# Kernel optimization log

Measured on AMD Instinct MI355X. Metric: run time of the kernel, lower is better.

The kernel has to match this reference:

```python
import jax, jax.numpy as jnp
import numpy as np
from jax import lax

R = 0.7          # ball-query radius
K = 32           # max neighbors per ball
STRIDE = 32      # spatial stride -> M = N // STRIDE anchors
COUT = 1024      # mlp_planes[0]


def fps(pts, M):
    """Furthest point sampling. pts: [N,3] -> int32 [M] indices (starts at 0, like CUDA FPS)."""
    N = pts.shape[0]

    def step(carry, _):
        d2, last = carry
        dist = jnp.sum((pts - pts[last]) ** 2, axis=-1)
        d2 = jnp.minimum(d2, dist)
        return (d2, jnp.argmax(d2).astype(jnp.int32)), last

    init = (jnp.full((N,), 1e10, dtype=pts.dtype), jnp.int32(0))
    _, idxs = lax.scan(step, init, None, length=M)
    return idxs


def ball_query(neigh, anchor):
    """neigh: [N,3], anchor: [M,3] -> int32 [M,K]: first K in-radius neighbor indices,
    padded with the first valid index (matching pointnet2 ball_query semantics)."""
    N = neigh.shape[0]
    d2 = jnp.sum((anchor[:, None, :] - neigh[None, :, :]) ** 2, axis=-1)  # [M,N]
    key = jnp.where(d2 < R * R, jnp.arange(N), N)  # valid points keep their position
    order = jnp.argsort(key, axis=-1)[:, :K]       # stable: first-in-order valid indices
    valid = jnp.take_along_axis(key, order, axis=-1) < N
    return jnp.where(valid, order, order[:, :1])


def setup_inputs() -> dict:
    key = jax.random.key(0)
    k1, k2 = jax.random.split(key)
    xyzs = jax.random.uniform(k1, (4, 16, 2048, 3), dtype=jnp.float32)  # points in unit cube
    w_d = jax.random.normal(k2, (COUT, 4), dtype=jnp.float32) * 0.1     # conv_d 1x1 weight
    return {"xyzs": xyzs, "w_d": w_d}


def reference(xyzs, w_d):
    B, T, N, _ = xyzs.shape
    M = N // STRIDE
    # replicate temporal padding [1,1]
    pad = jnp.concatenate([xyzs[:, :1], xyzs, xyzs[:, -1:]], axis=1)  # [B,T+2,N,3]

    anchors_src = pad[:, 1:-1].reshape(B * T, N, 3)
    aidx = jax.vmap(lambda p: fps(p, M))(anchors_src)                         # [BT,M]
    anchor = jnp.take_along_axis(anchors_src, aidx[..., None], axis=1)        # [BT,M,3]

    feat = None
    for dt in (-1, 0, 1):  # temporal kernel taps
        neigh = pad[:, 1 + dt: 1 + dt + T].reshape(B * T, N, 3)
        idx = jax.vmap(ball_query)(neigh, anchor)                             # [BT,M,K]
        grouped = jnp.take_along_axis(
            neigh, idx.reshape(B * T, M * K)[..., None], axis=1
        ).reshape(B * T, M, K, 3)
        disp = grouped - anchor[:, :, None, :]                                # xyz displacement
        d4 = jnp.concatenate(
            [disp, jnp.full((B * T, M, K, 1), float(dt), disp.dtype)], axis=-1
        )                                                                     # [BT,M,K,4]
        f = jax.nn.relu(jnp.einsum('nmkc,oc->nmko', d4, w_d))                 # 1x1 conv + ReLU
        f = jnp.max(f, axis=2)                                                # spatial max pool -> [BT,M,C]
        feat = f if feat is None else feat + f                                # temporal sum pool

    new_xyzs = anchor.reshape(B, T, M, 3)
    new_features = feat.reshape(B, T, M, COUT).transpose(0, 1, 3, 2)          # [B,T,C,M]
    return new_xyzs, new_features
```

## Files before the change

kernel.cpp:

```cpp
#include <hip/hip_runtime.h>
#include <hip/hip_fp16.h>

#define NB 4
#define NT 16
#define NN 2048
#define NM 64
#define NK 32
#define NC 1024

static __device__ inline __half2 h2max(__half2 a, __half2 b) {
    unsigned int ai = *(unsigned int*)&a, bi = *(unsigned int*)&b, di;
    asm("v_pk_max_f16 %0, %1, %2" : "=v"(di) : "v"(ai), "v"(bi));
    return *(__half2*)&di;
}

#define DPP_MAX_STEP(v, ctrl)                                                   \
    do {                                                                        \
        const int _mv = __builtin_amdgcn_update_dpp(                            \
            __float_as_int(v), __float_as_int(v), (ctrl), 0xf, 0xf, false);     \
        (v) = fmaxf((v), __int_as_float(_mv));                                  \
    } while (0)

static __device__ inline float readlane_f(float x, int l) {
    return __int_as_float(__builtin_amdgcn_readlane(__float_as_int(x), l));
}

__global__ __launch_bounds__(256) void fps_kernel(const float* __restrict__ xyzs,
                                                  float* __restrict__ out_xyz) {
    const int bt = blockIdx.x;
    const float* pts = xyzs + (size_t)bt * NN * 3;
    __shared__ unsigned long long sKey[2][4];
    __shared__ __align__(16) float sCand[2][4][4];
    __shared__ float sAnchor[NM * 3];
    __shared__ float sInit[3];
    const int tid = threadIdx.x;
    const int lane = tid & 63, wave = tid >> 6;
    float wpt[24];
    {
        const float4* pv = (const float4*)pts + (size_t)tid * 6;
        #pragma unroll
        for (int i = 0; i < 6; ++i) {
            const float4 f = pv[i];
            wpt[4 * i + 0] = f.x; wpt[4 * i + 1] = f.y; wpt[4 * i + 2] = f.z; wpt[4 * i + 3] = f.w;
        }
    }
    float px[8], py[8], pz[8], d2v[8];
    #pragma unroll
    for (int j = 0; j < 8; ++j) {
        px[j] = wpt[3 * j + 0]; py[j] = wpt[3 * j + 1]; pz[j] = wpt[3 * j + 2];
        d2v[j] = 1e10f;
    }
    if (tid == 0) { sInit[0] = px[0]; sInit[1] = py[0]; sInit[2] = pz[0]; }
    __syncthreads();
    float ax = sInit[0], ay = sInit[1], az = sInit[2];
    for (int it = 0; it < NM; ++it) {
        if (tid == 0) {
            sAnchor[it * 3 + 0] = ax; sAnchor[it * 3 + 1] = ay; sAnchor[it * 3 + 2] = az;
        }
        float bv = -1.0f; int bj = 0;
        #pragma unroll
        for (int j = 0; j < 8; ++j) {
            const float dx = __fsub_rn(px[j], ax), dy = __fsub_rn(py[j], ay), dz = __fsub_rn(pz[j], az);
            const float d = __fadd_rn(__fadd_rn(__fmul_rn(dx, dx), __fmul_rn(dy, dy)), __fmul_rn(dz, dz));
            d2v[j] = fminf(d2v[j], d);
            if (d2v[j] > bv) { bv = d2v[j]; bj = j; }
        }
        float v = bv;
        DPP_MAX_STEP(v, 0x111);
        DPP_MAX_STEP(v, 0x112);
        DPP_MAX_STEP(v, 0x114);
        DPP_MAX_STEP(v, 0x118);
        DPP_MAX_STEP(v, 0x142);
        DPP_MAX_STEP(v, 0x143);
        const float vmax = readlane_f(v, 63);
        const unsigned long long tied = __ballot(bv == vmax);
        const int src = (int)(__ffsll((long long)tied) - 1);
        const float cx0 = (bj & 1) ? px[1] : px[0], cx1 = (bj & 1) ? px[3] : px[2];
        const float cx2 = (bj & 1) ? px[5] : px[4], cx3 = (bj & 1) ? px[7] : px[6];
        const float cy0 = (bj & 1) ? py[1] : py[0], cy1 = (bj & 1) ? py[3] : py[2];
        const float cy2 = (bj & 1) ? py[5] : py[4], cy3 = (bj & 1) ? py[7] : py[6];
        const float cz0 = (bj & 1) ? pz[1] : pz[0], cz1 = (bj & 1) ? pz[3] : pz[2];
        const float cz2 = (bj & 1) ? pz[5] : pz[4], cz3 = (bj & 1) ? pz[7] : pz[6];
        const float cxa = (bj & 2) ? cx1 : cx0, cxb = (bj & 2) ? cx3 : cx2;
        const float cya = (bj & 2) ? cy1 : cy0, cyb = (bj & 2) ? cy3 : cy2;
        const float cza = (bj & 2) ? cz1 : cz0, czb = (bj & 2) ? cz3 : cz2;
        const float cx = (bj & 4) ? cxb : cxa;
        const float cy = (bj & 4) ? cyb : cya;
        const float cz = (bj & 4) ? czb : cza;
        const int idx = tid * 8 + bj;
        const int widx = __builtin_amdgcn_readlane(idx, src);
        const float wx = readlane_f(cx, src);
        const float wy = readlane_f(cy, src);
        const float wz = readlane_f(cz, src);
        const int par = it & 1;
        if (lane == 0) {
            sKey[par][wave] = ((unsigned long long)__float_as_uint(vmax) << 32)
                            | (unsigned)(NN - 1 - widx);
            *(float4*)&sCand[par][wave][0] = make_float4(wx, wy, wz, 0.0f);
        }
        __syncthreads();
        unsigned long long bk = sKey[par][0];
        float4 bc = *(const float4*)&sCand[par][0][0];
        #pragma unroll
        for (int i = 1; i < 4; ++i) {
            const unsigned long long ki = sKey[par][i];
            const float4 ci = *(const float4*)&sCand[par][i][0];
            if (ki > bk) { bk = ki; bc = ci; }
        }
        ax = bc.x; ay = bc.y; az = bc.z;
    }
    __syncthreads();
    for (int i = tid; i < NM * 3; i += 256)
        out_xyz[bt * NM * 3 + i] = sAnchor[i];
}

__global__ __launch_bounds__(256) void bq_kernel(const float* __restrict__ xyzs,
                                                 const float* __restrict__ anchors,
                                                 unsigned int* __restrict__ disp) {
    const int tid = threadIdx.x;
    const int lane = tid & 63, w = tid >> 6;
    const int q = blockIdx.x * 4 + w;
    const int bt = q / (NM * 3);
    const int r = q - bt * (NM * 3);
    const int m = r / 3, tap = r - m * 3;
    const int b = bt >> 4, t = bt & 15;
    __shared__ float sD[4][3][NK];
    const float ax = anchors[(bt * NM + m) * 3 + 0];
    const float ay = anchors[(bt * NM + m) * 3 + 1];
    const float az = anchors[(bt * NM + m) * 3 + 2];
    int tsrc = t + tap - 1;
    tsrc = tsrc < 0 ? 0 : (tsrc > NT - 1 ? NT - 1 : tsrc);
    const float* npts = xyzs + ((size_t)(b * NT + tsrc)) * NN * 3;
    int cnt = 0;
    for (int rr = 0; rr < NN / 64 && cnt < NK; ++rr) {
        const int n = rr * 64 + lane;
        const float dx = __fsub_rn(npts[n * 3 + 0], ax);
        const float dy = __fsub_rn(npts[n * 3 + 1], ay);
        const float dz = __fsub_rn(npts[n * 3 + 2], az);
        const float d2v = __fadd_rn(__fadd_rn(__fmul_rn(dx, dx), __fmul_rn(dy, dy)), __fmul_rn(dz, dz));
        const bool valid = d2v < 0.49f;
        const unsigned long long mask = __ballot(valid);
        const int pos = cnt + (int)__popcll(mask & ((1ull << lane) - 1ull));
        if (valid && pos < NK) {
            sD[w][0][pos] = dx; sD[w][1][pos] = dy; sD[w][2][pos] = dz;
        }
        cnt += (int)__popcll(mask);
    }
    if (cnt < NK) {
        float fx, fy, fz;
        if (cnt > 0) {
            fx = sD[w][0][0]; fy = sD[w][1][0]; fz = sD[w][2][0];
        } else {
            fx = __fsub_rn(npts[0], ax); fy = __fsub_rn(npts[1], ay); fz = __fsub_rn(npts[2], az);
        }
        if (lane >= cnt && lane < NK) {
            sD[w][0][lane] = fx; sD[w][1][lane] = fy; sD[w][2][lane] = fz;
        }
    }
    if (lane < 48) {
        const int c = lane >> 4, j = lane & 15;
        const __half2 hv = __float22half2_rn(make_float2(sD[w][c][2 * j], sD[w][c][2 * j + 1]));
        disp[(size_t)q * 48 + lane] = *(const unsigned int*)&hv;
    }
}

__global__ __launch_bounds__(256, 8) void conv_kernel(const unsigned int* __restrict__ disp,
                                                      const float* __restrict__ wd,
                                                      float* __restrict__ feat) {
    const int blk = blockIdx.x;
    const int bt = blk >> 5;
    const int inner = blk & 31;
    const int mh = inner >> 2, cq = inner & 3;
    const int tid = threadIdx.x;
    const int lane = tid & 63, w = tid >> 6;
    const int m0 = mh * 8 + w * 2;
    const int c0 = cq * 256 + lane;
    __half2 wx[4], wy[4], wz[4]; float ww[4];
    #pragma unroll
    for (int r = 0; r < 4; ++r) {
        const float4 wv = ((const float4*)wd)[c0 + 64 * r];
        wx[r] = __float2half2_rn(wv.x);
        wy[r] = __float2half2_rn(wv.y);
        wz[r] = __float2half2_rn(wv.z);
        ww[r] = wv.w;
    }
    float acc[4][2];
    #pragma unroll
    for (int r = 0; r < 4; ++r) { acc[r][0] = 0.0f; acc[r][1] = 0.0f; }

    #pragma unroll
    for (int mi = 0; mi < 2; ++mi) {
        #pragma unroll
        for (int tap = 0; tap < 3; ++tap) {
            const uint4* dp = (const uint4*)(disp + ((size_t)((bt * NM + m0 + mi) * 3 + tap)) * 48);
            __half2 a[4];
            #pragma unroll
            for (int h = 0; h < 2; ++h) {
                const uint4 ux0 = dp[2 * h],     ux1 = dp[2 * h + 1];
                const uint4 uy0 = dp[4 + 2 * h], uy1 = dp[5 + 2 * h];
                const uint4 uz0 = dp[8 + 2 * h], uz1 = dp[9 + 2 * h];
                const unsigned int X[8] = {ux0.x, ux0.y, ux0.z, ux0.w, ux1.x, ux1.y, ux1.z, ux1.w};
                const unsigned int Y[8] = {uy0.x, uy0.y, uy0.z, uy0.w, uy1.x, uy1.y, uy1.z, uy1.w};
                const unsigned int Z[8] = {uz0.x, uz0.y, uz0.z, uz0.w, uz1.x, uz1.y, uz1.z, uz1.w};
                #pragma unroll
                for (int j = 0; j < 8; ++j) {
                    const __half2 hx = *(const __half2*)&X[j];
                    const __half2 hy = *(const __half2*)&Y[j];
                    const __half2 hz = *(const __half2*)&Z[j];
                    #pragma unroll
                    for (int r = 0; r < 4; ++r) {
                        const __half2 s = __hfma2(wx[r], hx, __hfma2(wy[r], hy, __hmul2(wz[r], hz)));
                        a[r] = (h == 0 && j == 0) ? s : h2max(a[r], s);
                    }
                }
            }
            const float dtf = (float)(tap - 1);
            #pragma unroll
            for (int r = 0; r < 4; ++r) {
                const float mx = fmaxf(__low2float(a[r]), __high2float(a[r]));
                acc[r][mi] += fmaxf(0.0f, mx + ww[r] * dtf);
            }
        }
    }
    #pragma unroll
    for (int r = 0; r < 4; ++r) {
        float* dst = feat + ((size_t)bt * NC + c0 + 64 * r) * NM + m0;
        *(float2*)dst = make_float2(acc[r][0], acc[r][1]);
    }
}

extern "C" void kernel_launch(void* const* d_in, const int* in_sizes, int n_in,
                              void* d_out, int out_size, void* d_ws, size_t ws_size,
                              hipStream_t stream) {
    const float* xyzs = (const float*)d_in[0];
    const float* wd   = (const float*)d_in[1];
    float* out_xyz = (float*)d_out;
    float* featp   = out_xyz + NB * NT * NM * 3;
    unsigned int* dispw = (unsigned int*)d_ws;
    hipLaunchKernelGGL(fps_kernel, dim3(NB * NT), dim3(256), 0, stream, xyzs, out_xyz);
    hipLaunchKernelGGL(bq_kernel, dim3(NB * NT * NM * 3 / 4), dim3(256), 0, stream,
                       xyzs, out_xyz, dispw);
    hipLaunchKernelGGL(conv_kernel, dim3(2048), dim3(256), 0, stream,
                       dispw, wd, featp);
}
```

Measured before the change: 132.6 us.

## Double-buffer displacement loads and give each wave four anchors in conv kernel

The conv kernel now handles 4 anchors per wave instead of 2, which halves the grid and amortises the weight loads. Displacement rows are software-pipelined through two register buffers so the next tap's loads are issued while the current tap is being computed. Output is written with float4 stores. Register pressure goes up, so the launch bounds drop to 3 blocks per CU, and the smaller grid lowers occupancy and parallelism.

```diff
diff --git a/kernel.cpp b/kernel.cpp
--- a/kernel.cpp
+++ b/kernel.cpp
@@ -164,16 +164,16 @@
     }
 }
 
-__global__ __launch_bounds__(256, 8) void conv_kernel(const unsigned int* __restrict__ disp,
+__global__ __launch_bounds__(256, 3) void conv_kernel(const unsigned int* __restrict__ disp,
                                                       const float* __restrict__ wd,
                                                       float* __restrict__ feat) {
     const int blk = blockIdx.x;
-    const int bt = blk >> 5;
-    const int inner = blk & 31;
+    const int bt = blk >> 4;
+    const int inner = blk & 15;
     const int mh = inner >> 2, cq = inner & 3;
     const int tid = threadIdx.x;
     const int lane = tid & 63, w = tid >> 6;
-    const int m0 = mh * 8 + w * 2;
+    const int m0 = mh * 16 + w * 4;
     const int c0 = cq * 256 + lane;
     __half2 wx[4], wy[4], wz[4]; float ww[4];
     #pragma unroll
@@ -184,48 +184,50 @@
         wz[r] = __float2half2_rn(wv.z);
         ww[r] = wv.w;
     }
-    float acc[4][2];
-    #pragma unroll
-    for (int r = 0; r < 4; ++r) { acc[r][0] = 0.0f; acc[r][1] = 0.0f; }
-
-    #pragma unroll
-    for (int mi = 0; mi < 2; ++mi) {
-        #pragma unroll
-        for (int tap = 0; tap < 3; ++tap) {
-            const uint4* dp = (const uint4*)(disp + ((size_t)((bt * NM + m0 + mi) * 3 + tap)) * 48);
-            __half2 a[4];
+    float acc[4][4];
+    #pragma unroll
+    for (int r = 0; r < 4; ++r)
+        #pragma unroll
+        for (int mi = 0; mi < 4; ++mi) acc[r][mi] = 0.0f;
+
+    const uint4* base = (const uint4*)(disp + (size_t)((bt * NM + m0) * 3) * 48);
+    uint4 bufA[12], bufB[12];
+    #pragma unroll
+    for (int i = 0; i < 12; ++i) bufA[i] = base[i];
+    #pragma unroll
+    for (int t = 0; t < 12; ++t) {
+        const uint4* cur = (t & 1) ? bufB : bufA;
+        uint4*       nxt = (t & 1) ? bufA : bufB;
+        if (t < 11) {
+            const uint4* np = base + (size_t)(t + 1) * 12;
             #pragma unroll
-            for (int h = 0; h < 2; ++h) {
-                const uint4 ux0 = dp[2 * h],     ux1 = dp[2 * h + 1];
-                const uint4 uy0 = dp[4 + 2 * h], uy1 = dp[5 + 2 * h];
-                const uint4 uz0 = dp[8 + 2 * h], uz1 = dp[9 + 2 * h];
-                const unsigned int X[8] = {ux0.x, ux0.y, ux0.z, ux0.w, ux1.x, ux1.y, ux1.z, ux1.w};
-                const unsigned int Y[8] = {uy0.x, uy0.y, uy0.z, uy0.w, uy1.x, uy1.y, uy1.z, uy1.w};
-                const unsigned int Z[8] = {uz0.x, uz0.y, uz0.z, uz0.w, uz1.x, uz1.y, uz1.z, uz1.w};
-                #pragma unroll
-                for (int j = 0; j < 8; ++j) {
-                    const __half2 hx = *(const __half2*)&X[j];
-                    const __half2 hy = *(const __half2*)&Y[j];
-                    const __half2 hz = *(const __half2*)&Z[j];
-                    #pragma unroll
-                    for (int r = 0; r < 4; ++r) {
-                        const __half2 s = __hfma2(wx[r], hx, __hfma2(wy[r], hy, __hmul2(wz[r], hz)));
-                        a[r] = (h == 0 && j == 0) ? s : h2max(a[r], s);
-                    }
-                }
-            }
-            const float dtf = (float)(tap - 1);
+            for (int i = 0; i < 12; ++i) nxt[i] = np[i];
+        }
+        const unsigned int* uw = (const unsigned int*)cur;
+        __half2 a[4];
+        #pragma unroll
+        for (int j = 0; j < 16; ++j) {
+            const __half2 hx = *(const __half2*)&uw[j];
+            const __half2 hy = *(const __half2*)&uw[16 + j];
+            const __half2 hz = *(const __half2*)&uw[32 + j];
             #pragma unroll
             for (int r = 0; r < 4; ++r) {
-                const float mx = fmaxf(__low2float(a[r]), __high2float(a[r]));
-                acc[r][mi] += fmaxf(0.0f, mx + ww[r] * dtf);
+                const __half2 s = __hfma2(wx[r], hx, __hfma2(wy[r], hy, __hmul2(wz[r], hz)));
+                a[r] = (j == 0) ? s : h2max(a[r], s);
             }
+        }
+        const int mi = t / 3, tap = t - mi * 3;
+        const float dtf = (float)(tap - 1);
+        #pragma unroll
+        for (int r = 0; r < 4; ++r) {
+            const float mx = fmaxf(__low2float(a[r]), __high2float(a[r]));
+            acc[r][mi] += fmaxf(0.0f, mx + ww[r] * dtf);
         }
     }
     #pragma unroll
     for (int r = 0; r < 4; ++r) {
         float* dst = feat + ((size_t)bt * NC + c0 + 64 * r) * NM + m0;
-        *(float2*)dst = make_float2(acc[r][0], acc[r][1]);
+        *(float4*)dst = make_float4(acc[r][0], acc[r][1], acc[r][2], acc[r][3]);
     }
 }
 
@@ -240,6 +242,6 @@
     hipLaunchKernelGGL(fps_kernel, dim3(NB * NT), dim3(256), 0, stream, xyzs, out_xyz);
     hipLaunchKernelGGL(bq_kernel, dim3(NB * NT * NM * 3 / 4), dim3(256), 0, stream,
                        xyzs, out_xyz, dispw);
-    hipLaunchKernelGGL(conv_kernel, dim3(2048), dim3(256), 0, stream,
+    hipLaunchKernelGGL(conv_kernel, dim3(1024), dim3(256), 0, stream,
                        dispw, wd, featp);
 }
```

Result: faster. 129.4 us (-2.4%).
